# Performance work log

Measured on AMD Instinct MI355X. Metric: run time of the kernel, lower is better.

The kernel has to match this reference:

```python
import jax, jax.numpy as jnp
import numpy as np

N = 65536   # total nodes
E = 262144  # total edges (before self loops)
B = 2048    # graphs in batch
H = 4       # attention heads
D = 192     # per-head dim (hidden_dim // heads)
HID = 768   # hidden dim
L = 2       # num layers
EPS = 1e-5
NEG_SLOPE = 0.2  # PyG GATConv leaky_relu slope


def setup_inputs() -> dict:
    key = jax.random.key(0)
    ks = jax.random.split(key, 10)
    s = 0.02
    x = jax.random.normal(ks[0], (N, HID), dtype=jnp.float32)
    edge_index = jax.random.randint(ks[1], (2, E), 0, N)
    batch_vec = jnp.sort(jax.random.randint(ks[2], (N,), 0, B))
    W = jax.random.normal(ks[3], (L, HID, HID), dtype=jnp.float32) * s
    att_src = jax.random.normal(ks[4], (L, H, D), dtype=jnp.float32) * s
    att_dst = jax.random.normal(ks[5], (L, H, D), dtype=jnp.float32) * s
    bias = jnp.zeros((L, HID), dtype=jnp.float32)
    ln_gamma = jnp.ones((L, HID), dtype=jnp.float32)
    ln_beta = jnp.zeros((L, HID), dtype=jnp.float32)
    out_w = jax.random.normal(ks[6], (HID, HID), dtype=jnp.float32) * s
    out_b = jnp.zeros((HID,), dtype=jnp.float32)
    return dict(x=x, edge_index=edge_index, batch_vec=batch_vec, W=W,
                att_src=att_src, att_dst=att_dst, bias=bias,
                ln_gamma=ln_gamma, ln_beta=ln_beta, out_w=out_w, out_b=out_b)


def _gat_layer(x, src, dst, W_l, a_src, a_dst, b_l):
    # x: [N, HID] -> projected per-head features [N, H, D]
    xw = (x @ W_l).reshape(N, H, D)
    alpha_src = jnp.einsum('nhd,hd->nh', xw, a_src)  # [N, H]
    alpha_dst = jnp.einsum('nhd,hd->nh', xw, a_dst)  # [N, H]
    # edge attention logits (message j->i uses alpha_src[j] + alpha_dst[i])
    e = jax.nn.leaky_relu(alpha_src[src] + alpha_dst[dst], NEG_SLOPE)  # [E2, H]
    # segment softmax over incoming edges per destination node (self loops
    # guarantee every node has >= 1 incoming edge)
    m = jax.ops.segment_max(e, dst, num_segments=N)
    ex = jnp.exp(e - m[dst])
    denom = jax.ops.segment_sum(ex, dst, num_segments=N)
    alpha = ex / denom[dst]                                            # [E2, H]
    # attention-weighted scatter aggregation
    out = jax.ops.segment_sum(alpha[:, :, None] * xw[src], dst, num_segments=N)
    return out.reshape(N, HID) + b_l


def reference(x, edge_index, batch_vec, W, att_src, att_dst, bias,
              ln_gamma, ln_beta, out_w, out_b):
    loops = jnp.arange(N)
    src = jnp.concatenate([edge_index[0], loops])  # add_self_loops=True
    dst = jnp.concatenate([edge_index[1], loops])
    h = x
    for l in range(L):
        out = _gat_layer(h, src, dst, W[l], att_src[l], att_dst[l], bias[l])
        mu = jnp.mean(out, axis=-1, keepdims=True)
        var = jnp.var(out, axis=-1, keepdims=True)
        out = (out - mu) * jax.lax.rsqrt(var + EPS) * ln_gamma[l] + ln_beta[l]
        out = jax.nn.relu(out)
        h = out + h  # residual (in_dim == hidden_dim for every layer)
    # global mean pool over graphs
    ones = jnp.ones((N,), h.dtype)
    cnt = jax.ops.segment_sum(ones, batch_vec, num_segments=B)
    h_g = jax.ops.segment_sum(h, batch_vec, num_segments=B)
    h_g = h_g / jnp.maximum(cnt, 1.0)[:, None]
    return h_g @ out_w + out_b
```

## Files before the change

kernel.cpp:

```cpp
#include <hip/hip_runtime.h>
#include <hip/hip_bf16.h>

constexpr int NN  = 65536;
constexpr int EE  = 262144;
constexpr int E2  = EE + NN;
constexpr int BB  = 2048;
constexpr int HH  = 4;
constexpr int DD  = 192;
constexpr int HD  = 768;
constexpr int LL  = 2;
constexpr float EPS = 1e-5f;
constexpr float SLOPE = 0.2f;

typedef __attribute__((ext_vector_type(8))) short short8;
typedef __attribute__((ext_vector_type(4))) float f32x4;
typedef __hip_bfloat16 bf16;

__global__ void zero_k(float* __restrict__ p, int n) {
    int i = blockIdx.x * 256 + threadIdx.x;
    if (i < n) p[i] = 0.f;
}

__global__ void conv_k(const float4* __restrict__ src, bf16* __restrict__ dst, int n4) {
    int i = blockIdx.x * 256 + threadIdx.x;
    if (i >= n4) return;
    float4 v = src[i];
    bf16* o = dst + (size_t)i * 4;
    o[0] = __float2bfloat16(v.x); o[1] = __float2bfloat16(v.y);
    o[2] = __float2bfloat16(v.z); o[3] = __float2bfloat16(v.w);
}

__global__ __launch_bounds__(256) void wconv3_k(const float* __restrict__ W,
                                                const float* __restrict__ OW,
                                                bf16* __restrict__ Wt3) {
    __shared__ float tile[32][33];
    const float* src = (blockIdx.z < 2) ? (W + (size_t)blockIdx.z * HD * HD) : OW;
    bf16* dst = Wt3 + (size_t)blockIdx.z * HD * HD;
    int bx = blockIdx.x * 32;
    int by = blockIdx.y * 32;
    int tx = threadIdx.x & 31, ty = threadIdx.x >> 5;
    #pragma unroll
    for (int r = 0; r < 32; r += 8)
        tile[ty + r][tx] = src[(size_t)(by + ty + r) * HD + bx + tx];
    __syncthreads();
    #pragma unroll
    for (int r = 0; r < 32; r += 8)
        dst[(size_t)(bx + ty + r) * HD + by + tx] = __float2bfloat16(tile[tx][ty + r]);
}

__device__ __forceinline__ void load16_lds(const void* g, void* l) {
    __builtin_amdgcn_global_load_lds(
        (const __attribute__((address_space(1))) unsigned int*)g,
        (__attribute__((address_space(3))) unsigned int*)l, 16, 0, 0);
}

__global__ __launch_bounds__(512, 2) void gemm256_k(
    const bf16* __restrict__ A, const bf16* __restrict__ Bt, bf16* __restrict__ C)
{
    constexpr int K  = HD;
    constexpr int NT = K / 32;

    __shared__ __attribute__((aligned(16))) char smem[4 * 32768];

    int bid  = blockIdx.x;
    int flat = (bid & 7) * 96 + (bid >> 3);
    int by   = flat / 3;
    int bx   = flat - by * 3;
    int bm   = by * 256, bn = bx * 256;

    int tid  = threadIdx.x;
    int wid  = tid >> 6, lane = tid & 63;
    int wr   = wid >> 2, wc = wid & 3;
    int m16  = lane & 15, quad = lane >> 4;

    int prow = ((tid >> 6) << 4) | (tid & 15);
    int slot = (tid >> 4) & 3;
    const bf16* gA = A  + (size_t)(bm + prow) * K + slot * 8;
    const bf16* gB = Bt + (size_t)(bn + prow) * K + slot * 8;
    char* ldst = smem + tid * 16;

    auto STAGE1 = [&](int t, int k) {
        char* d = ldst + (size_t)(t & 3) * 32768 + k * 8192;
        const bf16* s = ((k < 2) ? gA : gB) + (size_t)t * 32
                      + ((k & 1) ? (size_t)128 * K : 0);
        load16_lds(s, d);
    };

    f32x4 acc[8][4];
    #pragma unroll
    for (int i = 0; i < 8; i++)
        #pragma unroll
        for (int j = 0; j < 4; j++) acc[i][j] = (f32x4)0.f;

    auto TILE2PH = [&](const char* ab, int ts) {
        const char* bb = ab + 16384;
        short8 a[8], b[4];
        #pragma unroll
        for (int m = 0; m < 8; ++m)
            a[m] = *(const short8*)(ab + (wr * 8 + m) * 1024 + lane * 16);
        b[0] = *(const short8*)(bb + (wc * 4 + 0) * 1024 + lane * 16);
        b[1] = *(const short8*)(bb + (wc * 4 + 1) * 1024 + lane * 16);
        if (ts >= 0) { STAGE1(ts, 0); STAGE1(ts, 1); }
        __builtin_amdgcn_s_barrier();
        asm volatile("s_waitcnt lgkmcnt(0)" ::: "memory");
        __builtin_amdgcn_s_setprio(1);
        #pragma unroll
        for (int m = 0; m < 8; ++m) {
            acc[m][0] = __builtin_amdgcn_mfma_f32_16x16x32_bf16(a[m], b[0], acc[m][0], 0, 0, 0);
            acc[m][1] = __builtin_amdgcn_mfma_f32_16x16x32_bf16(a[m], b[1], acc[m][1], 0, 0, 0);
        }
        __builtin_amdgcn_s_setprio(0);
        __builtin_amdgcn_s_barrier();
        b[2] = *(const short8*)(bb + (wc * 4 + 2) * 1024 + lane * 16);
        b[3] = *(const short8*)(bb + (wc * 4 + 3) * 1024 + lane * 16);
        if (ts >= 0) { STAGE1(ts, 2); STAGE1(ts, 3); }
        __builtin_amdgcn_s_barrier();
        asm volatile("s_waitcnt lgkmcnt(0)" ::: "memory");
        __builtin_amdgcn_s_setprio(1);
        #pragma unroll
        for (int m = 0; m < 8; ++m) {
            acc[m][2] = __builtin_amdgcn_mfma_f32_16x16x32_bf16(a[m], b[2], acc[m][2], 0, 0, 0);
            acc[m][3] = __builtin_amdgcn_mfma_f32_16x16x32_bf16(a[m], b[3], acc[m][3], 0, 0, 0);
        }
        __builtin_amdgcn_s_setprio(0);
        if (ts >= 0) asm volatile("s_waitcnt vmcnt(4)" ::: "memory");
        else         asm volatile("s_waitcnt vmcnt(0)" ::: "memory");
        __builtin_amdgcn_s_barrier();
    };

    #pragma unroll
    for (int k = 0; k < 4; ++k) STAGE1(0, k);
    #pragma unroll
    for (int k = 0; k < 4; ++k) STAGE1(1, k);
    asm volatile("s_waitcnt vmcnt(0)" ::: "memory");
    __builtin_amdgcn_s_barrier();

    for (int i = 0; i < NT / 2; ++i) {
        int t  = 2 * i;
        int ts = (i < NT / 2 - 1) ? t + 2 : -1;
        TILE2PH(smem + (size_t)(t & 3) * 32768,       ts);
        TILE2PH(smem + (size_t)((t + 1) & 3) * 32768, (ts >= 0) ? ts + 1 : -1);
    }

    #pragma unroll
    for (int m = 0; m < 8; ++m) {
        int row0 = bm + wr * 128 + m * 16 + quad * 4;
        #pragma unroll
        for (int n = 0; n < 4; ++n) {
            int col = bn + wc * 64 + n * 16 + m16;
            #pragma unroll
            for (int r = 0; r < 4; ++r)
                C[(size_t)(row0 + r) * HD + col] = __float2bfloat16(acc[m][n][r]);
        }
    }
}

template <bool BF16_OUT, bool SWIZ>
__global__ __launch_bounds__(256) void gemm_bf16_k(
    const bf16* __restrict__ A, const bf16* __restrict__ Bt,
    float* __restrict__ Cf, bf16* __restrict__ Cb, const float* __restrict__ bias)
{
    constexpr int K = HD;
    __shared__ __attribute__((aligned(16))) short As[128 * 32];
    __shared__ __attribute__((aligned(16))) short Bs[128 * 32];

    int bx, by;
    if (SWIZ) {
        int gid = blockIdx.x;
        int xcd = gid & 7, lid = gid >> 3;
        int sg = lid / 48, sl = lid - sg * 48;
        by = (xcd << 6) + (sg << 3) + (sl & 7);
        bx = sl >> 3;
    } else {
        bx = blockIdx.x; by = blockIdx.y;
    }

    int tid  = threadIdx.x;
    int wave = tid >> 6, lane = tid & 63;
    int wy = wave >> 1, wx = wave & 1;
    int m16 = lane & 15, quad = lane >> 4;
    int bm = by * 128;
    int bn = bx * 128;

    int p0 = wave * 128 + lane;
    int r0 = p0 >> 2, c0 = p0 & 3;
    int p1 = p0 + 64;
    int r1 = p1 >> 2, c1 = p1 & 3;

    const bf16* gA0 = A  + (size_t)(bm + r0) * K + c0 * 8;
    const bf16* gA1 = A  + (size_t)(bm + r1) * K + c1 * 8;
    const bf16* gB0 = Bt + (size_t)(bn + r0) * K + c0 * 8;
    const bf16* gB1 = Bt + (size_t)(bn + r1) * K + c1 * 8;

    f32x4 acc[4][4];
    #pragma unroll
    for (int i = 0; i < 4; i++)
        #pragma unroll
        for (int j = 0; j < 4; j++) acc[i][j] = (f32x4)0.f;

    const short8* Ac = (const short8*)As;
    const short8* Bc = (const short8*)Bs;

    for (int k0 = 0; k0 < K; k0 += 32) {
        load16_lds(gA0 + k0, &As[p0 * 8]);
        load16_lds(gA1 + k0, &As[p1 * 8]);
        load16_lds(gB0 + k0, &Bs[p0 * 8]);
        load16_lds(gB1 + k0, &Bs[p1 * 8]);
        __syncthreads();

        short8 a[4], b[4];
        #pragma unroll
        for (int i = 0; i < 4; i++)
            a[i] = Ac[(wy * 64 + i * 16 + m16) * 4 + quad];
        #pragma unroll
        for (int j = 0; j < 4; j++)
            b[j] = Bc[(wx * 64 + j * 16 + m16) * 4 + quad];
        #pragma unroll
        for (int i = 0; i < 4; i++)
            #pragma unroll
            for (int j = 0; j < 4; j++)
                acc[i][j] = __builtin_amdgcn_mfma_f32_16x16x32_bf16(a[i], b[j], acc[i][j], 0, 0, 0);
        __syncthreads();
    }

    #pragma unroll
    for (int j = 0; j < 4; j++) {
        int col = bn + wx * 64 + j * 16 + m16;
        float badd = (!BF16_OUT && bias) ? bias[col] : 0.f;
        #pragma unroll
        for (int i = 0; i < 4; i++) {
            int row0 = bm + wy * 64 + i * 16 + quad * 4;
            #pragma unroll
            for (int r = 0; r < 4; r++) {
                if (BF16_OUT)
                    Cb[(size_t)(row0 + r) * HD + col] = __float2bfloat16(acc[i][j][r]);
                else
                    Cf[(size_t)(row0 + r) * HD + col] = acc[i][j][r] + badd;
            }
        }
    }
}

__device__ __forceinline__ float bflo(unsigned u) { return __uint_as_float(u << 16); }
__device__ __forceinline__ float bfhi(unsigned u) { return __uint_as_float(u & 0xffff0000u); }

__global__ __launch_bounds__(256) void alpha_k(
    const bf16* __restrict__ xw,
    const float* __restrict__ asl, const float* __restrict__ adl,
    float* __restrict__ asrc, float* __restrict__ adst)
{
    int wave = threadIdx.x >> 6, lane = threadIdx.x & 63;
    int n = blockIdx.x * 4 + wave;
    int c = lane * 12;

    const bf16* row = xw + (size_t)n * HD + c;
    uint2 u0 = *(const uint2*)(row);
    uint2 u1 = *(const uint2*)(row + 4);
    uint2 u2 = *(const uint2*)(row + 8);
    float v[12] = {bflo(u0.x), bfhi(u0.x), bflo(u0.y), bfhi(u0.y),
                   bflo(u1.x), bfhi(u1.x), bflo(u1.y), bfhi(u1.y),
                   bflo(u2.x), bfhi(u2.x), bflo(u2.y), bfhi(u2.y)};

    float4 a0 = *(const float4*)(asl + c);
    float4 a1 = *(const float4*)(asl + c + 4);
    float4 a2 = *(const float4*)(asl + c + 8);
    float4 d0 = *(const float4*)(adl + c);
    float4 d1 = *(const float4*)(adl + c + 4);
    float4 d2 = *(const float4*)(adl + c + 8);
    float aa[12] = {a0.x,a0.y,a0.z,a0.w,a1.x,a1.y,a1.z,a1.w,a2.x,a2.y,a2.z,a2.w};
    float dd[12] = {d0.x,d0.y,d0.z,d0.w,d1.x,d1.y,d1.z,d1.w,d2.x,d2.y,d2.z,d2.w};

    float s1 = 0.f, s2 = 0.f;
    #pragma unroll
    for (int k = 0; k < 12; k++) { s1 += v[k] * aa[k]; s2 += v[k] * dd[k]; }

    #pragma unroll
    for (int off = 1; off < 16; off <<= 1) {
        s1 += __shfl_xor(s1, off, 64);
        s2 += __shfl_xor(s2, off, 64);
    }
    if ((lane & 15) == 0) {
        int head = lane >> 4;
        asrc[(size_t)n * HH + head] = s1;
        adst[(size_t)n * HH + head] = s2;
    }
}

__global__ void hist_k(const int* __restrict__ ei, int* __restrict__ deg) {
    int e = blockIdx.x * 256 + threadIdx.x;
    int dst = (e < EE) ? ei[EE + e] : (e - EE);
    atomicAdd(&deg[dst], 1);
}

__global__ void scan1_k(const int* __restrict__ deg, int* __restrict__ incl,
                        int* __restrict__ blocksum) {
    __shared__ int s[256];
    int t = threadIdx.x, n = blockIdx.x * 256 + t;
    int v = deg[n];
    s[t] = v;
    for (int off = 1; off < 256; off <<= 1) {
        __syncthreads();
        int tmp = (t >= off) ? s[t - off] : 0;
        __syncthreads();
        s[t] += tmp;
    }
    incl[n] = s[t];
    if (t == 255) blocksum[blockIdx.x] = s[255];
}

__global__ void scan2_k(const int* __restrict__ blocksum, int* __restrict__ blockoff) {
    __shared__ int s[256];
    int t = threadIdx.x;
    int v = blocksum[t];
    s[t] = v;
    for (int off = 1; off < 256; off <<= 1) {
        __syncthreads();
        int tmp = (t >= off) ? s[t - off] : 0;
        __syncthreads();
        s[t] += tmp;
    }
    blockoff[t] = s[t] - v;
}

__global__ void scan3_k(const int* __restrict__ deg, const int* __restrict__ blockoff,
                        int* __restrict__ incl_cursor, int* __restrict__ rowstart) {
    int t = threadIdx.x, n = blockIdx.x * 256 + t;
    int rs = blockoff[blockIdx.x] + incl_cursor[n] - deg[n];
    rowstart[n] = rs;
    incl_cursor[n] = rs;
    if (n == 0) rowstart[NN] = E2;
}

__global__ void fill_k(const int* __restrict__ ei, int* __restrict__ cursor,
                       int* __restrict__ csr_src) {
    int e = blockIdx.x * 256 + threadIdx.x;
    int src = (e < EE) ? ei[e] : (e - EE);
    int dst = (e < EE) ? ei[EE + e] : (e - EE);
    int pos = atomicAdd(&cursor[dst], 1);
    csr_src[pos] = src;
}

__global__ __launch_bounds__(256) void agg_k(
    const bf16* __restrict__ xw, const float4* __restrict__ asrc,
    const float4* __restrict__ adst, const int* __restrict__ rowstart,
    const int* __restrict__ csr_src,
    const float* __restrict__ bias_l, const float* __restrict__ gamma_l,
    const float* __restrict__ beta_l, const bf16* __restrict__ h_in,
    bf16* __restrict__ h_out)
{
    __shared__ float s_w[4][64][4];
    __shared__ int   s_src[4][64];

    int wave = threadIdx.x >> 6, lane = threadIdx.x & 63;
    int i = blockIdx.x * 4 + wave;
    int c = lane * 12;
    int myhead = lane >> 4;

    int r0 = rowstart[i], r1 = rowstart[i + 1];
    float4 ad = adst[i];

    float acc[12];
    #pragma unroll
    for (int k = 0; k < 12; k++) acc[k] = 0.f;
    float4 den = make_float4(0.f, 0.f, 0.f, 0.f);

    for (int base = r0; base < r1; base += 64) {
        int cnt = min(64, r1 - base);
        float4 w4 = make_float4(0.f, 0.f, 0.f, 0.f);
        if (lane < cnt) {
            int s = csr_src[base + lane];
            s_src[wave][lane] = s;
            float4 a = asrc[s];
            float t0 = a.x + ad.x; t0 = (t0 > 0.f) ? t0 : SLOPE * t0;
            float t1 = a.y + ad.y; t1 = (t1 > 0.f) ? t1 : SLOPE * t1;
            float t2 = a.z + ad.z; t2 = (t2 > 0.f) ? t2 : SLOPE * t2;
            float t3 = a.w + ad.w; t3 = (t3 > 0.f) ? t3 : SLOPE * t3;
            w4 = make_float4(__expf(t0), __expf(t1), __expf(t2), __expf(t3));
            *(float4*)&s_w[wave][lane][0] = w4;
        }
        den.x += w4.x; den.y += w4.y; den.z += w4.z; den.w += w4.w;
        for (int e = 0; e < cnt; e++) {
            int src = __builtin_amdgcn_readfirstlane(s_src[wave][e]);
            float wv = s_w[wave][e][myhead];
            const bf16* row = xw + (size_t)src * HD + c;
            uint2 u0 = *(const uint2*)(row);
            uint2 u1 = *(const uint2*)(row + 4);
            uint2 u2 = *(const uint2*)(row + 8);
            acc[0] += wv * bflo(u0.x); acc[1]  += wv * bfhi(u0.x);
            acc[2] += wv * bflo(u0.y); acc[3]  += wv * bfhi(u0.y);
            acc[4] += wv * bflo(u1.x); acc[5]  += wv * bfhi(u1.x);
            acc[6] += wv * bflo(u1.y); acc[7]  += wv * bfhi(u1.y);
            acc[8] += wv * bflo(u2.x); acc[9]  += wv * bfhi(u2.x);
            acc[10] += wv * bflo(u2.y); acc[11] += wv * bfhi(u2.y);
        }
    }

    #pragma unroll
    for (int off = 32; off > 0; off >>= 1) {
        den.x += __shfl_xor(den.x, off, 64);
        den.y += __shfl_xor(den.y, off, 64);
        den.z += __shfl_xor(den.z, off, 64);
        den.w += __shfl_xor(den.w, off, 64);
    }
    float deni = (myhead == 0) ? den.x : (myhead == 1) ? den.y
               : (myhead == 2) ? den.z : den.w;
    float inv = 1.f / deni;

    float4 b0 = *(const float4*)(bias_l + c);
    float4 b1 = *(const float4*)(bias_l + c + 4);
    float4 b2 = *(const float4*)(bias_l + c + 8);
    float v[12];
    v[0] = acc[0] * inv + b0.x; v[1]  = acc[1] * inv + b0.y;
    v[2] = acc[2] * inv + b0.z; v[3]  = acc[3] * inv + b0.w;
    v[4] = acc[4] * inv + b1.x; v[5]  = acc[5] * inv + b1.y;
    v[6] = acc[6] * inv + b1.z; v[7]  = acc[7] * inv + b1.w;
    v[8] = acc[8] * inv + b2.x; v[9]  = acc[9] * inv + b2.y;
    v[10] = acc[10] * inv + b2.z; v[11] = acc[11] * inv + b2.w;

    float s = 0.f;
    #pragma unroll
    for (int k = 0; k < 12; k++) s += v[k];
    #pragma unroll
    for (int off = 32; off > 0; off >>= 1) s += __shfl_xor(s, off, 64);
    float mean = s * (1.f / (float)HD);

    float q = 0.f;
    #pragma unroll
    for (int k = 0; k < 12; k++) { float d = v[k] - mean; q += d * d; }
    #pragma unroll
    for (int off = 32; off > 0; off >>= 1) q += __shfl_xor(q, off, 64);
    float rs = rsqrtf(q * (1.f / (float)HD) + EPS);

    float4 g0 = *(const float4*)(gamma_l + c);
    float4 g1 = *(const float4*)(gamma_l + c + 4);
    float4 g2 = *(const float4*)(gamma_l + c + 8);
    float4 e0 = *(const float4*)(beta_l + c);
    float4 e1 = *(const float4*)(beta_l + c + 4);
    float4 e2 = *(const float4*)(beta_l + c + 8);
    float gg[12] = {g0.x,g0.y,g0.z,g0.w,g1.x,g1.y,g1.z,g1.w,g2.x,g2.y,g2.z,g2.w};
    float bb[12] = {e0.x,e0.y,e0.z,e0.w,e1.x,e1.y,e1.z,e1.w,e2.x,e2.y,e2.z,e2.w};

    const bf16* hrow = h_in + (size_t)i * HD + c;
    uint2 hu0 = *(const uint2*)(hrow);
    uint2 hu1 = *(const uint2*)(hrow + 4);
    uint2 hu2 = *(const uint2*)(hrow + 8);
    float hres[12] = {bflo(hu0.x), bfhi(hu0.x), bflo(hu0.y), bfhi(hu0.y),
                      bflo(hu1.x), bfhi(hu1.x), bflo(hu1.y), bfhi(hu1.y),
                      bflo(hu2.x), bfhi(hu2.x), bflo(hu2.y), bfhi(hu2.y)};

    bf16 pk[12];
    #pragma unroll
    for (int k = 0; k < 12; k++) {
        float o = fmaxf((v[k] - mean) * rs * gg[k] + bb[k], 0.f) + hres[k];
        pk[k] = __float2bfloat16(o);
    }
    bf16* orow = h_out + (size_t)i * HD + c;
    *(uint2*)(orow)     = *(const uint2*)&pk[0];
    *(uint2*)(orow + 4) = *(const uint2*)&pk[4];
    *(uint2*)(orow + 8) = *(const uint2*)&pk[8];
}

__global__ __launch_bounds__(192) void pool_k(
    const bf16* __restrict__ h, const int* __restrict__ bv,
    bf16* __restrict__ hg)
{
    int g = blockIdx.x, t = threadIdx.x;
    int lo = 0, hi = NN;
    while (lo < hi) { int mid = (lo + hi) >> 1; if (bv[mid] < g) lo = mid + 1; else hi = mid; }
    int start = lo;
    hi = NN;
    while (lo < hi) { int mid = (lo + hi) >> 1; if (bv[mid] < g + 1) lo = mid + 1; else hi = mid; }
    int end = lo;
    int c = t * 4;
    float a0 = 0.f, a1 = 0.f, a2 = 0.f, a3 = 0.f;
    for (int n = start; n < end; n++) {
        uint2 u = *(const uint2*)(h + (size_t)n * HD + c);
        a0 += bflo(u.x); a1 += bfhi(u.x); a2 += bflo(u.y); a3 += bfhi(u.y);
    }
    float sc = 1.f / fmaxf((float)(end - start), 1.f);
    bf16 pk[4];
    pk[0] = __float2bfloat16(a0 * sc); pk[1] = __float2bfloat16(a1 * sc);
    pk[2] = __float2bfloat16(a2 * sc); pk[3] = __float2bfloat16(a3 * sc);
    *(uint2*)(hg + (size_t)g * HD + c) = *(const uint2*)pk;
}

extern "C" void kernel_launch(void* const* d_in, const int* in_sizes, int n_in,
                              void* d_out, int out_size, void* d_ws, size_t ws_size,
                              hipStream_t stream)
{
    (void)in_sizes; (void)n_in; (void)out_size; (void)ws_size;
    const float* x       = (const float*)d_in[0];
    const int*   ei      = (const int*)d_in[1];
    const int*   bv      = (const int*)d_in[2];
    const float* W       = (const float*)d_in[3];
    const float* att_src = (const float*)d_in[4];
    const float* att_dst = (const float*)d_in[5];
    const float* bias    = (const float*)d_in[6];
    const float* gamma   = (const float*)d_in[7];
    const float* beta    = (const float*)d_in[8];
    const float* out_w   = (const float*)d_in[9];
    const float* out_b   = (const float*)d_in[10];
    float* out = (float*)d_out;

    char* p = (char*)d_ws;
    size_t off = 0;
    auto take = [&](size_t bytes) -> char* {
        char* r = p + off;
        off = (off + bytes + 255) & ~(size_t)255;
        return r;
    };
    bf16* xw        = (bf16*)take((size_t)NN * HD * 2);
    bf16* hbf0      = (bf16*)take((size_t)NN * HD * 2);
    bf16* hbf1      = (bf16*)take((size_t)NN * HD * 2);
    bf16* Wt3       = (bf16*)take((size_t)3 * HD * HD * 2);
    float* asrc     = (float*)take((size_t)NN * HH * 4);
    float* adst     = (float*)take((size_t)NN * HH * 4);
    int*   deg      = (int*)take((size_t)NN * 4);
    int*   rowstart = (int*)take((size_t)(NN + 1) * 4);
    int*   cursor   = (int*)take((size_t)NN * 4);
    int*   blocksum = (int*)take(256 * 4);
    int*   blockoff = (int*)take(256 * 4);
    int*   csr_src  = (int*)take((size_t)E2 * 4);
    bf16*  hg       = (bf16*)take((size_t)BB * HD * 2);

    const int EB = E2 / 256;

    zero_k<<<NN / 256, 256, 0, stream>>>((float*)deg, NN);
    hist_k<<<EB, 256, 0, stream>>>(ei, deg);
    scan1_k<<<NN / 256, 256, 0, stream>>>(deg, cursor, blocksum);
    scan2_k<<<1, 256, 0, stream>>>(blocksum, blockoff);
    scan3_k<<<NN / 256, 256, 0, stream>>>(deg, blockoff, cursor, rowstart);
    fill_k<<<EB, 256, 0, stream>>>(ei, cursor, csr_src);

    conv_k<<<(NN * HD / 4 + 255) / 256, 256, 0, stream>>>((const float4*)x, hbf0, NN * HD / 4);
    wconv3_k<<<dim3(HD / 32, HD / 32, 3), 256, 0, stream>>>(W, out_w, Wt3);

    bf16* hin = hbf0;
    bf16* hout = hbf1;
    for (int l = 0; l < LL; l++) {
        gemm256_k<<<768, 512, 0, stream>>>(hin, Wt3 + (size_t)l * HD * HD, xw);
        alpha_k<<<NN / 4, 256, 0, stream>>>(xw, att_src + (size_t)l * HH * DD,
                                            att_dst + (size_t)l * HH * DD, asrc, adst);
        agg_k<<<NN / 4, 256, 0, stream>>>(xw, (const float4*)asrc, (const float4*)adst,
                                          rowstart, csr_src,
                                          bias + (size_t)l * HD, gamma + (size_t)l * HD,
                                          beta + (size_t)l * HD, hin, hout);
        bf16* tmp = hin; hin = hout; hout = tmp;
    }

    pool_k<<<BB, 192, 0, stream>>>(hin, bv, hg);
    gemm_bf16_k<false, false><<<dim3(HD / 128, BB / 128), 256, 0, stream>>>(
        hg, Wt3 + (size_t)2 * HD * HD, out, nullptr, out_b);
}
```

Before: 829.6 us.

## Process four edges per wave in parallel in GAT aggregation

Restructures the aggregation kernel so each wave splits into four 16-lane groups. Each group handles a different edge at the same time, and each lane loads 48 contiguous bf16 values with 16-byte loads instead of 12 values with 8-byte loads. The goal is to raise memory-level parallelism and cut the serial per-edge loop trip count. The partial sums are combined with cross-group shuffles, and LayerNorm statistics are computed over the 16-lane replicated sums. In exchange the kernel needs 48 accumulators per lane, which raises register pressure, and launch bounds now request at least 3 blocks per CU.

```diff
diff --git a/kernel.cpp b/kernel.cpp
--- a/kernel.cpp
+++ b/kernel.cpp
@@ -340,7 +340,7 @@
     csr_src[pos] = src;
 }
 
-__global__ __launch_bounds__(256) void agg_k(
+__global__ __launch_bounds__(256, 3) void agg_k(
     const bf16* __restrict__ xw, const float4* __restrict__ asrc,
     const float4* __restrict__ adst, const int* __restrict__ rowstart,
     const int* __restrict__ csr_src,
@@ -353,16 +353,24 @@
 
     int wave = threadIdx.x >> 6, lane = threadIdx.x & 63;
     int i = blockIdx.x * 4 + wave;
-    int c = lane * 12;
-    int myhead = lane >> 4;
+    int q = lane & 15;
+    int grp = lane >> 4;
+    int head = q >> 2;
+    int cb = q * 48;
 
     int r0 = rowstart[i], r1 = rowstart[i + 1];
     float4 ad = adst[i];
 
-    float acc[12];
-    #pragma unroll
-    for (int k = 0; k < 12; k++) acc[k] = 0.f;
+    float acc[48];
+    #pragma unroll
+    for (int k = 0; k < 48; k++) acc[k] = 0.f;
     float4 den = make_float4(0.f, 0.f, 0.f, 0.f);
+
+#define ACC8(U, O) \
+    acc[(O)+0] += wv * bflo(U.x); acc[(O)+1] += wv * bfhi(U.x); \
+    acc[(O)+2] += wv * bflo(U.y); acc[(O)+3] += wv * bfhi(U.y); \
+    acc[(O)+4] += wv * bflo(U.z); acc[(O)+5] += wv * bfhi(U.z); \
+    acc[(O)+6] += wv * bflo(U.w); acc[(O)+7] += wv * bfhi(U.w);
 
     for (int base = r0; base < r1; base += 64) {
         int cnt = min(64, r1 - base);
@@ -379,20 +387,30 @@
             *(float4*)&s_w[wave][lane][0] = w4;
         }
         den.x += w4.x; den.y += w4.y; den.z += w4.z; den.w += w4.w;
-        for (int e = 0; e < cnt; e++) {
-            int src = __builtin_amdgcn_readfirstlane(s_src[wave][e]);
-            float wv = s_w[wave][e][myhead];
-            const bf16* row = xw + (size_t)src * HD + c;
-            uint2 u0 = *(const uint2*)(row);
-            uint2 u1 = *(const uint2*)(row + 4);
-            uint2 u2 = *(const uint2*)(row + 8);
-            acc[0] += wv * bflo(u0.x); acc[1]  += wv * bfhi(u0.x);
-            acc[2] += wv * bflo(u0.y); acc[3]  += wv * bfhi(u0.y);
-            acc[4] += wv * bflo(u1.x); acc[5]  += wv * bfhi(u1.x);
-            acc[6] += wv * bflo(u1.y); acc[7]  += wv * bfhi(u1.y);
-            acc[8] += wv * bflo(u2.x); acc[9]  += wv * bfhi(u2.x);
-            acc[10] += wv * bflo(u2.y); acc[11] += wv * bfhi(u2.y);
+
+        for (int eb = 0; eb < cnt; eb += 4) {
+            int e = eb + grp;
+            if (e < cnt) {
+                int src  = s_src[wave][e];
+                float wv = s_w[wave][e][head];
+                const bf16* row = xw + (size_t)src * HD + cb;
+                uint4 u0 = *(const uint4*)(row);
+                uint4 u1 = *(const uint4*)(row + 8);
+                uint4 u2 = *(const uint4*)(row + 16);
+                uint4 u3 = *(const uint4*)(row + 24);
+                uint4 u4 = *(const uint4*)(row + 32);
+                uint4 u5 = *(const uint4*)(row + 40);
+                ACC8(u0, 0);  ACC8(u1, 8);  ACC8(u2, 16);
+                ACC8(u3, 24); ACC8(u4, 32); ACC8(u5, 40);
+            }
         }
+    }
+#undef ACC8
+
+    #pragma unroll
+    for (int k = 0; k < 48; k++) {
+        acc[k] += __shfl_xor(acc[k], 16, 64);
+        acc[k] += __shfl_xor(acc[k], 32, 64);
     }
 
     #pragma unroll
@@ -402,45 +420,68 @@
         den.z += __shfl_xor(den.z, off, 64);
         den.w += __shfl_xor(den.w, off, 64);
     }
-    float deni = (myhead == 0) ? den.x : (myhead == 1) ? den.y
-               : (myhead == 2) ? den.z : den.w;
+    float deni = (head == 0) ? den.x : (head == 1) ? den.y
+               : (head == 2) ? den.z : den.w;
     float inv = 1.f / deni;
 
-    float4 b0 = *(const float4*)(bias_l + c);
-    float4 b1 = *(const float4*)(bias_l + c + 4);
-    float4 b2 = *(const float4*)(bias_l + c + 8);
-    float v[12];
-    v[0] = acc[0] * inv + b0.x; v[1]  = acc[1] * inv + b0.y;
-    v[2] = acc[2] * inv + b0.z; v[3]  = acc[3] * inv + b0.w;
-    v[4] = acc[4] * inv + b1.x; v[5]  = acc[5] * inv + b1.y;
-    v[6] = acc[6] * inv + b1.z; v[7]  = acc[7] * inv + b1.w;
-    v[8] = acc[8] * inv + b2.x; v[9]  = acc[9] * inv + b2.y;
-    v[10] = acc[10] * inv + b2.z; v[11] = acc[11] * inv + b2.w;
-
-    float s = 0.f;
-    #pragma unroll
-    for (int k = 0; k < 12; k++) s += v[k];
-    #pragma unroll
-    for (int off = 32; off > 0; off >>= 1) s += __shfl_xor(s, off, 64);
+    float sa = 0.f;
+    #pragma unroll
+    for (int k = 0; k < 48; k++) sa += acc[k];
+    float sb = 0.f;
+    #pragma unroll
+    for (int j = 0; j < 12; j++) {
+        float4 b = *(const float4*)(bias_l + cb + 4 * j);
+        sb += b.x + b.y + b.z + b.w;
+    }
+    float s = sa * inv + sb;
+    #pragma unroll
+    for (int off = 1; off < 16; off <<= 1) s += __shfl_xor(s, off, 64);
     float mean = s * (1.f / (float)HD);
 
-    float q = 0.f;
-    #pragma unroll
-    for (int k = 0; k < 12; k++) { float d = v[k] - mean; q += d * d; }
-    #pragma unroll
-    for (int off = 32; off > 0; off >>= 1) q += __shfl_xor(q, off, 64);
-    float rs = rsqrtf(q * (1.f / (float)HD) + EPS);
-
-    float4 g0 = *(const float4*)(gamma_l + c);
-    float4 g1 = *(const float4*)(gamma_l + c + 4);
-    float4 g2 = *(const float4*)(gamma_l + c + 8);
-    float4 e0 = *(const float4*)(beta_l + c);
-    float4 e1 = *(const float4*)(beta_l + c + 4);
-    float4 e2 = *(const float4*)(beta_l + c + 8);
-    float gg[12] = {g0.x,g0.y,g0.z,g0.w,g1.x,g1.y,g1.z,g1.w,g2.x,g2.y,g2.z,g2.w};
-    float bb[12] = {e0.x,e0.y,e0.z,e0.w,e1.x,e1.y,e1.z,e1.w,e2.x,e2.y,e2.z,e2.w};
-
-    const bf16* hrow = h_in + (size_t)i * HD + c;
+    float qv = 0.f;
+    #pragma unroll
+    for (int j = 0; j < 12; j++) {
+        float4 b = *(const float4*)(bias_l + cb + 4 * j);
+        float d0 = acc[4*j+0] * inv + b.x - mean;
+        float d1 = acc[4*j+1] * inv + b.y - mean;
+        float d2 = acc[4*j+2] * inv + b.z - mean;
+        float d3 = acc[4*j+3] * inv + b.w - mean;
+        qv += d0*d0 + d1*d1 + d2*d2 + d3*d3;
+    }
+    #pragma unroll
+    for (int off = 1; off < 16; off <<= 1) qv += __shfl_xor(qv, off, 64);
+    float rs = rsqrtf(qv * (1.f / (float)HD) + EPS);
+
+    float astrip[12];
+    if (grp == 0) {
+        #pragma unroll
+        for (int k = 0; k < 12; k++) astrip[k] = acc[k];
+    } else if (grp == 1) {
+        #pragma unroll
+        for (int k = 0; k < 12; k++) astrip[k] = acc[12 + k];
+    } else if (grp == 2) {
+        #pragma unroll
+        for (int k = 0; k < 12; k++) astrip[k] = acc[24 + k];
+    } else {
+        #pragma unroll
+        for (int k = 0; k < 12; k++) astrip[k] = acc[36 + k];
+    }
+    int cs = cb + grp * 12;
+
+    float4 b0 = *(const float4*)(bias_l + cs);
+    float4 b1 = *(const float4*)(bias_l + cs + 4);
+    float4 b2 = *(const float4*)(bias_l + cs + 8);
+    float bbv[12] = {b0.x,b0.y,b0.z,b0.w,b1.x,b1.y,b1.z,b1.w,b2.x,b2.y,b2.z,b2.w};
+    float4 g0 = *(const float4*)(gamma_l + cs);
+    float4 g1 = *(const float4*)(gamma_l + cs + 4);
+    float4 g2 = *(const float4*)(gamma_l + cs + 8);
+    float ggv[12] = {g0.x,g0.y,g0.z,g0.w,g1.x,g1.y,g1.z,g1.w,g2.x,g2.y,g2.z,g2.w};
+    float4 e0 = *(const float4*)(beta_l + cs);
+    float4 e1 = *(const float4*)(beta_l + cs + 4);
+    float4 e2 = *(const float4*)(beta_l + cs + 8);
+    float eev[12] = {e0.x,e0.y,e0.z,e0.w,e1.x,e1.y,e1.z,e1.w,e2.x,e2.y,e2.z,e2.w};
+
+    const bf16* hrow = h_in + (size_t)i * HD + cs;
     uint2 hu0 = *(const uint2*)(hrow);
     uint2 hu1 = *(const uint2*)(hrow + 4);
     uint2 hu2 = *(const uint2*)(hrow + 8);
@@ -451,10 +492,11 @@
     bf16 pk[12];
     #pragma unroll
     for (int k = 0; k < 12; k++) {
-        float o = fmaxf((v[k] - mean) * rs * gg[k] + bb[k], 0.f) + hres[k];
+        float vk = astrip[k] * inv + bbv[k];
+        float o  = fmaxf((vk - mean) * rs * ggv[k] + eev[k], 0.f) + hres[k];
         pk[k] = __float2bfloat16(o);
     }
-    bf16* orow = h_out + (size_t)i * HD + c;
+    bf16* orow = h_out + (size_t)i * HD + cs;
     *(uint2*)(orow)     = *(const uint2*)&pk[0];
     *(uint2*)(orow + 4) = *(const uint2*)&pk[4];
     *(uint2*)(orow + 8) = *(const uint2*)&pk[8];
```

Measured after the change: 946.6 us. 14.1% more time.
